# Optimization experiments

Hardware: AMD Instinct MI355X
Metric: run time of the kernel (lower is better)

Reference implementation:

```python
import jax, jax.numpy as jnp
import numpy as np

N_NODES = 20000
N_EDGES = 480000
NUM_BATCH = 8     # B = batch_id.max()+1 (static)
NUM_GLOBAL = 3    # virtual_frame_num default
NUM_RBF = 16
EPS = 1e-20


def make_frames(n, ca, c):
    """OpenFold Rigid.make_transform_from_reference. Returns (R [N,3,3], t [N,3])."""
    nl = n - ca
    cl = c - ca
    cx, cy, cz = cl[:, 0], cl[:, 1], cl[:, 2]
    norm1 = jnp.sqrt(EPS + cx * cx + cy * cy)
    s1, c1 = -cy / norm1, cx / norm1
    norm2 = jnp.sqrt(EPS + cx * cx + cy * cy + cz * cz)
    s2, c2 = cz / norm2, jnp.sqrt(cx * cx + cy * cy) / norm2
    z = jnp.zeros_like(c1)
    o = jnp.ones_like(c1)
    R1 = jnp.stack([jnp.stack([c1, -s1, z], -1),
                    jnp.stack([s1, c1, z], -1),
                    jnp.stack([z, z, o], -1)], -2)          # rot about z
    R2 = jnp.stack([jnp.stack([c2, z, s2], -1),
                    jnp.stack([z, o, z], -1),
                    jnp.stack([-s2, z, c2], -1)], -2)       # rot about y
    Rc = jnp.einsum('nij,njk->nik', R2, R1)
    nr = jnp.einsum('nij,nj->ni', Rc, nl)
    ny, nz = nr[:, 1], nr[:, 2]
    norm3 = jnp.sqrt(EPS + ny * ny + nz * nz)
    sn, cn = -nz / norm3, ny / norm3
    Rn = jnp.stack([jnp.stack([o, z, z], -1),
                    jnp.stack([z, cn, -sn], -1),
                    jnp.stack([z, sn, cn], -1)], -2)        # rot about x
    R = jnp.einsum('nij,njk->nik', Rn, Rc).swapaxes(-1, -2)
    return R, ca


def rbf_encode(D):
    # D_min=0, D_max=20, 16 bins (matches rbf_func)
    mu = jnp.linspace(0.0, 20.0, NUM_RBF, dtype=D.dtype)
    sigma = 20.0 / NUM_RBF
    z = (D[..., None] - mu) / sigma
    return jnp.exp(-z * z)


def decouple(U):
    # safe norm: exact forward, NaN-free backward at U==0
    sq = jnp.sum(U * U, axis=-1, keepdims=True)
    norm = jnp.where(sq == 0, 0.0, jnp.sqrt(jnp.where(sq == 0, 1.0, sq)))
    direct = U / (norm + 1e-6)
    return jnp.concatenate([direct, rbf_encode(norm[..., 0])], axis=-1)


def int_embedding(d, num_embeddings):
    freq = jnp.exp(jnp.arange(0, num_embeddings, 2, dtype=jnp.float32)
                   * (-np.log(10000.0) / num_embeddings))
    ang = d[:, None].astype(jnp.float32) * freq[None, :]
    return jnp.concatenate([jnp.cos(ang), jnp.sin(ang)], -1)


def forward(X, edge_idx, batch_id, chain_encoding):
    N = X.shape[0]
    src, dst = edge_idx[0], edge_idx[1]
    R, t = make_frames(X[:, 0], X[:, 1], X[:, 2])
    # T_ts = T[dst].invert().compose(T[src]):  R_dst^T R_src,  R_dst^T (t_src - t_dst)
    R_ts = jnp.einsum('eji,ejk->eik', R[dst], R[src])
    t_ts = jnp.einsum('eji,ej->ei', R[dst], t[src] - t[dst])
    # --- node features ---
    diffX = jnp.diff(X.reshape(-1, 3), axis=0)
    diffX = jnp.concatenate([jnp.zeros((1, 3), X.dtype), diffX], 0).reshape(N, 4, 3)
    diffX_proj = jnp.einsum('nji,naj->nai', R, diffX)   # R^T @ diffX
    V = decouple(diffX_proj).reshape(N, -1)             # [N, 4*(3+16)=76]
    V = jnp.where(jnp.isnan(V), 0.0, V)
    # --- edge features ---
    atoms = jnp.concatenate([X[src], X[dst]], axis=1)   # [E,8,3]
    diffE = jnp.einsum('eji,eaj->eai', R[src], atoms - t[src][:, None, :])
    diffE = decouple(diffE).reshape(src.shape[0], -1)   # [E,152]
    pos_embed = int_embedding(src - dst, 16)            # [E,16]
    E_quant = R_ts.swapaxes(-1, -2).reshape(-1, 9)      # inverted rot mats
    E_trans = decouple(t_ts)                            # [E,19]
    Efeat = jnp.concatenate([diffE, E_quant, E_trans, pos_embed], -1)  # [E,196]
    # --- virtual (global) frames ---
    B, G = NUM_BATCH, NUM_GLOBAL
    g_src = jnp.concatenate([batch_id + N + k * B for k in range(G)])  # [G*N]
    g_dst = jnp.tile(jnp.arange(N, dtype=edge_idx.dtype), G)
    edge_idx_g = jnp.concatenate([jnp.stack([g_src, g_dst]),
                                  jnp.stack([g_dst, g_src])], axis=1)  # [2, 2*G*N]
    batch_id_g = jnp.tile(jnp.arange(B, dtype=batch_id.dtype), G)      # [G*B]
    h_V_g = jnp.tile(jnp.arange(G), B)                                 # [G*B]
    V_g = int_embedding(h_V_g, V.shape[-1]).astype(V.dtype)            # [G*B,76]
    n_ge = edge_idx_g.shape[1]
    E_g = jnp.zeros((n_ge, Efeat.shape[1]), Efeat.dtype)
    eye = jnp.eye(3, dtype=X.dtype)
    # --- merge local + global ---
    V_all = jnp.concatenate([V, V_g], 0)
    E_all = jnp.concatenate([Efeat, E_g], 0)
    R_all = jnp.concatenate([R, jnp.broadcast_to(eye, (G * B, 3, 3))], 0)
    t_all = jnp.concatenate([t, jnp.zeros((G * B, 3), X.dtype)], 0)
    Rts_all = jnp.concatenate([R_ts, jnp.broadcast_to(eye, (n_ge, 3, 3))], 0)
    tts_all = jnp.concatenate([t_ts, jnp.zeros((n_ge, 3), X.dtype)], 0)
    batch_all = jnp.concatenate([batch_id, batch_id_g])
    edge_all = jnp.concatenate([edge_idx, edge_idx_g], axis=1)
    chain_all = jnp.concatenate([chain_encoding, jnp.ones_like(batch_id_g) + 1000])
    return V_all, E_all, R_all, t_all, Rts_all, tts_all, batch_all, edge_all, chain_all


def setup_inputs() -> dict:
    key = jax.random.key(0)
    k1, k2, k3, k4 = jax.random.split(key, 4)
    X = jax.random.normal(k1, (N_NODES, 4, 3), dtype=jnp.float32)
    edge_idx = jax.random.randint(k2, (2, N_EDGES), 0, N_NODES, dtype=jnp.int32)
    batch_id = jnp.sort(jax.random.randint(k3, (N_NODES,), 0, NUM_BATCH, dtype=jnp.int32))
    chain_encoding = jax.random.randint(k4, (N_NODES,), 0, 10, dtype=jnp.int32)
    return {"X": X, "edge_idx": edge_idx, "batch_id": batch_id,
            "chain_encoding": chain_encoding}


def reference(X, edge_idx, batch_id, chain_encoding):
    return forward(X, edge_idx, batch_id, chain_encoding)
```

## Files before the change

kernel.cpp:

```cpp
#include <hip/hip_runtime.h>

#define NN 20000
#define NE 480000

#define OFF_V    0
#define OFF_E    1521824
#define OFF_R    119121824
#define OFF_T    119302040
#define OFF_RTS  119362112
#define OFF_TTS  124762112
#define OFF_BAT  126562112
#define OFF_EDG  126582136
#define OFF_CHN  127782136

#define REC 65

struct Frame { float m[3][3]; float t[3]; };

__device__ __forceinline__ void make_frame(const float a0[3], const float a1[3],
                                           const float a2[3], Frame& F){
  float nlx = a0[0]-a1[0], nly = a0[1]-a1[1], nlz = a0[2]-a1[2];
  float cx  = a2[0]-a1[0], cy  = a2[1]-a1[1], cz  = a2[2]-a1[2];
  float xy2 = cx*cx + cy*cy;
  float n1 = sqrtf(1e-20f + xy2);
  float s1 = -cy/n1, c1 = cx/n1;
  float n2 = sqrtf(1e-20f + xy2 + cz*cz);
  float s2 = cz/n2, c2 = sqrtf(xy2)/n2;
  float R00 = c2*c1, R01 = -c2*s1, R02 = s2;
  float R10 = s1,    R11 = c1,     R12 = 0.f;
  float R20 = -s2*c1,R21 = s2*s1,  R22 = c2;
  float nr1 = R10*nlx + R11*nly + R12*nlz;
  float nr2 = R20*nlx + R21*nly + R22*nlz;
  float n3 = sqrtf(1e-20f + nr1*nr1 + nr2*nr2);
  float sn = -nr2/n3, cn = nr1/n3;
  F.m[0][0]=R00;              F.m[0][1]=R01;              F.m[0][2]=R02;
  F.m[1][0]=cn*R10 - sn*R20;  F.m[1][1]=cn*R11 - sn*R21;  F.m[1][2]=cn*R12 - sn*R22;
  F.m[2][0]=sn*R10 + cn*R20;  F.m[2][1]=sn*R11 + cn*R21;  F.m[2][2]=sn*R12 + cn*R22;
  F.t[0]=a1[0]; F.t[1]=a1[1]; F.t[2]=a1[2];
}

__device__ __forceinline__ void group4(float ux, float uy, float uz, float* rec, int off){
  float sq = ux*ux + uy*uy + uz*uz;
  float nrm = (sq == 0.f) ? 0.f : sqrtf(sq);
  float inv = 1.0f / (nrm + 1e-6f);
  rec[off+0] = ux*inv; rec[off+1] = uy*inv; rec[off+2] = uz*inv; rec[off+3] = nrm;
}

__global__ __launch_bounds__(128) void edge_kernel(
    const float* __restrict__ X, const int* __restrict__ ei,
    float* __restrict__ out){
  __shared__ float lds[2*64*REC];
  const int tid  = threadIdx.x;
  const int lane = tid & 63;
  const int wave = tid >> 6;
  const int e_my = blockIdx.x*128 + tid;

  int src = ei[e_my], dst = ei[NE + e_my];
  const float* ps = X + (size_t)src*12;
  const float* pd = X + (size_t)dst*12;
  float as[4][3], ad[4][3];
#pragma unroll
  for (int i = 0; i < 12; i++){ as[i/3][i%3] = ps[i]; ad[i/3][i%3] = pd[i]; }
  Frame Fs, Fd;
  make_frame(as[0], as[1], as[2], Fs);
  make_frame(ad[0], ad[1], ad[2], Fd);

  float* rec = lds + (wave*64 + lane)*REC;

#pragma unroll
  for (int q = 0; q < 4; q++){
    float y0 = as[q][0]-Fs.t[0], y1 = as[q][1]-Fs.t[1], y2 = as[q][2]-Fs.t[2];
    group4(Fs.m[0][0]*y0 + Fs.m[0][1]*y1 + Fs.m[0][2]*y2,
           Fs.m[1][0]*y0 + Fs.m[1][1]*y1 + Fs.m[1][2]*y2,
           Fs.m[2][0]*y0 + Fs.m[2][1]*y1 + Fs.m[2][2]*y2, rec, 4*q);
  }
#pragma unroll
  for (int q = 0; q < 4; q++){
    float y0 = ad[q][0]-Fs.t[0], y1 = ad[q][1]-Fs.t[1], y2 = ad[q][2]-Fs.t[2];
    group4(Fs.m[0][0]*y0 + Fs.m[0][1]*y1 + Fs.m[0][2]*y2,
           Fs.m[1][0]*y0 + Fs.m[1][1]*y1 + Fs.m[1][2]*y2,
           Fs.m[2][0]*y0 + Fs.m[2][1]*y1 + Fs.m[2][2]*y2, rec, 16 + 4*q);
  }
#pragma unroll
  for (int i = 0; i < 3; i++)
#pragma unroll
    for (int k = 0; k < 3; k++)
      rec[36+3*i+k] = Fd.m[i][0]*Fs.m[k][0] + Fd.m[i][1]*Fs.m[k][1] + Fd.m[i][2]*Fs.m[k][2];
  {
    float d0 = Fs.t[0]-Fd.t[0], d1 = Fs.t[1]-Fd.t[1], d2 = Fs.t[2]-Fd.t[2];
    float t0 = Fd.m[0][0]*d0 + Fd.m[0][1]*d1 + Fd.m[0][2]*d2;
    float t1 = Fd.m[1][0]*d0 + Fd.m[1][1]*d1 + Fd.m[1][2]*d2;
    float t2 = Fd.m[2][0]*d0 + Fd.m[2][1]*d1 + Fd.m[2][2]*d2;
    rec[45] = t0; rec[46] = t1; rec[47] = t2;
    group4(t0, t1, t2, rec, 32);
  }
  {
    float df = (float)(src - dst);
    const float FR[8] = {1.f, 0.31622776601683794f, 0.1f, 0.031622776601683794f,
                         0.01f, 0.0031622776601683794f, 0.001f, 0.00031622776601683794f};
#pragma unroll
    for (int k = 0; k < 8; k++){
      float s, c; __sincosf(df * FR[k], &s, &c);
      rec[48+k] = c; rec[56+k] = s;
    }
  }
  out[OFF_EDG + e_my]          = (float)src;
  out[OFF_EDG + 600000 + e_my] = (float)dst;

  __syncthreads();

  int   offb[4];
  float msk[4], mu[4];
#pragma unroll
  for (int c = 0; c < 4; c++){
    int j = 4*lane + c;
    int off = 0; float m = 0.f, rm = 0.f;
    if (j < 152){
      int jj = (j < 76) ? j : j - 76;
      int g  = ((j < 76) ? 0 : 4) + jj/19;
      int r  = jj - 19*(jj/19);
      if (r < 3) off = 4*g + r;
      else { off = 4*g + 3; m = 1.f; rm = (float)(r-3) * (20.0f/15.0f); }
    } else if (j < 161){
      int q = j - 152;
      off = 36 + 3*(q - 3*(q/3)) + q/3;
    } else if (j < 180){
      int r = j - 161;
      if (r < 3) off = 32 + r;
      else { off = 35; m = 1.f; rm = (float)(r-3) * (20.0f/15.0f); }
    } else if (j < 196){
      off = 48 + (j - 180);
    } else {
      off = 0;
    }
    offb[c] = off; msk[c] = m; mu[c] = rm;
  }

  const float* wlds = lds + wave*64*REC;
  const int wave_ebase = blockIdx.x*128 + wave*64;
  float4* pstore = reinterpret_cast<float4*>(out + OFF_E + (size_t)wave_ebase*196) + lane;

#pragma unroll 2
  for (int e = 0; e < 64; e++){
    const float* r = wlds + e*REC;
    float v[4];
#pragma unroll
    for (int c = 0; c < 4; c++){
      float x  = r[offb[c]];
      float z  = (x - mu[c]) * 0.8f;
      float rv = __expf(-z*z);
      v[c] = fmaf(msk[c], rv - x, x);
    }
    if (lane < 49)
      *pstore = make_float4(v[0], v[1], v[2], v[3]);
    pstore += 49;
  }

#pragma unroll
  for (int k = 0; k < 9; k++){
    int f = k*64 + lane;
    int e = f/9, m = f - 9*e;
    out[OFF_RTS + (size_t)wave_ebase*9 + f] = wlds[e*REC + 36 + m];
  }
#pragma unroll
  for (int k = 0; k < 3; k++){
    int f = k*64 + lane;
    int e = f/3, m = f - 3*e;
    out[OFF_TTS + (size_t)wave_ebase*3 + f] = wlds[e*REC + 45 + m];
  }
}

__device__ __forceinline__ void decouple19(float ux, float uy, float uz, float* b){
  float sq = ux*ux + uy*uy + uz*uz;
  float nrm = (sq == 0.f) ? 0.f : sqrtf(sq);
  float inv = 1.0f / (nrm + 1e-6f);
  b[0] = ux*inv; b[1] = uy*inv; b[2] = uz*inv;
#pragma unroll
  for (int k = 0; k < 16; k++){
    float mu = (float)k * (20.0f/15.0f);
    float z = (nrm - mu) * 0.8f;
    b[3+k] = __expf(-z*z);
  }
}

__global__ __launch_bounds__(256) void node_kernel(
    const float* __restrict__ X, const int* __restrict__ bat,
    const int* __restrict__ chn, float* __restrict__ out){
  int n = blockIdx.x*256 + threadIdx.x;
  if (n >= NN) return;
  const float* xp = X + (size_t)n*12;
  float a[4][3];
#pragma unroll
  for (int i = 0; i < 12; i++) a[i/3][i%3] = xp[i];
  Frame F; make_frame(a[0], a[1], a[2], F);

  float d[4][3];
  if (n > 0){ d[0][0]=a[0][0]-xp[-3]; d[0][1]=a[0][1]-xp[-2]; d[0][2]=a[0][2]-xp[-1]; }
  else      { d[0][0]=0.f; d[0][1]=0.f; d[0][2]=0.f; }
#pragma unroll
  for (int q = 1; q < 4; q++){
    d[q][0]=a[q][0]-a[q-1][0]; d[q][1]=a[q][1]-a[q-1][1]; d[q][2]=a[q][2]-a[q-1][2];
  }

  float buf[76];
#pragma unroll
  for (int q = 0; q < 4; q++){
    float vx = F.m[0][0]*d[q][0] + F.m[0][1]*d[q][1] + F.m[0][2]*d[q][2];
    float vy = F.m[1][0]*d[q][0] + F.m[1][1]*d[q][1] + F.m[1][2]*d[q][2];
    float vz = F.m[2][0]*d[q][0] + F.m[2][1]*d[q][1] + F.m[2][2]*d[q][2];
    decouple19(vx, vy, vz, buf + q*19);
  }
  float4* vrow = reinterpret_cast<float4*>(out + OFF_V + (size_t)n*76);
#pragma unroll
  for (int i = 0; i < 19; i++)
    vrow[i] = make_float4(buf[4*i], buf[4*i+1], buf[4*i+2], buf[4*i+3]);

  float* rr = out + OFF_R + (size_t)n*9;
#pragma unroll
  for (int i = 0; i < 3; i++)
#pragma unroll
    for (int j = 0; j < 3; j++) rr[3*i+j] = F.m[j][i];

  float* tr = out + OFF_T + (size_t)n*3;
#pragma unroll
  for (int i = 0; i < 3; i++) tr[i] = F.t[i];

  out[OFF_BAT + n] = (float)bat[n];
  out[OFF_CHN + n] = (float)chn[n];
}

__global__ __launch_bounds__(256) void fill_kernel(const int* __restrict__ bat,
                                                   float* __restrict__ out){
  int i = blockIdx.x*256 + threadIdx.x;
  if (i < 5880000){
    uint4 z; z.x=0; z.y=0; z.z=0; z.w=0;
    reinterpret_cast<uint4*>(out + 95601824)[i] = z;
    return;
  }
  i -= 5880000;
  if (i < 90000){
    uint4 z; z.x=0; z.y=0; z.z=0; z.w=0;
    reinterpret_cast<uint4*>(out + 126202112)[i] = z;
    return;
  }
  i -= 90000;
  if (i < 1080000){
    int r = i % 9;
    out[OFF_RTS + 4320000 + i] = (r==0 || r==4 || r==8) ? 1.0f : 0.0f;
    return;
  }
  i -= 1080000;
  if (i < 120000){
    int v0, v1;
    if (i < 60000){ int k = i/20000, m = i - 20000*k; v0 = bat[m] + 20000 + k*8; v1 = m; }
    else { int i2 = i - 60000; int k = i2/20000, m = i2 - 20000*k; v0 = m; v1 = bat[m] + 20000 + k*8; }
    out[OFF_EDG + 480000 + i]          = (float)v0;
    out[OFF_EDG + 600000 + 480000 + i] = (float)v1;
    return;
  }
  i -= 120000;
  if (i >= 2160) return;
  if (i < 1824){
    int r = i / 76, c = i % 76;
    float hv = (float)(r % 3);
    int j = (c < 38) ? c : c - 38;
    float fr = __expf(-(float)(2*j) * (9.210340371976184f/76.0f));
    float ang = hv * fr;
    out[OFF_V + 1520000 + i] = (c < 38) ? cosf(ang) : sinf(ang);
  } else if (i < 2040){
    int k = i - 1824; int r = k % 9;
    out[OFF_R + 180000 + k] = (r==0 || r==4 || r==8) ? 1.0f : 0.0f;
  } else if (i < 2112){
    out[OFF_T + 60000 + (i - 2040)] = 0.0f;
  } else if (i < 2136){
    int k = i - 2112;
    out[OFF_BAT + 20000 + k] = (float)(k % 8);
  } else {
    out[OFF_CHN + 20000 + (i - 2136)] = 1001.0f;
  }
}

extern "C" void kernel_launch(void* const* d_in, const int* in_sizes, int n_in,
                              void* d_out, int out_size, void* d_ws, size_t ws_size,
                              hipStream_t stream) {
  const float* X   = (const float*)d_in[0];
  const int* ei    = (const int*)d_in[1];
  const int* bat   = (const int*)d_in[2];
  const int* chn   = (const int*)d_in[3];
  float* out = (float*)d_out;

  node_kernel<<<(NN + 255)/256, 256, 0, stream>>>(X, bat, chn, out);
  edge_kernel<<<NE/128, 128, 0, stream>>>(X, ei, out);
  fill_kernel<<<(7172160 + 255)/256, 256, 0, stream>>>(bat, out);
}
```

Measured before the change: 120.6 us.

## Fuse node, edge and fill kernels into a single block-dispatched launch

Merges the three separate kernels into one mega kernel that selects edge, node or fill work by block index, removing two launches and the gaps between them. The fill path now writes two uint4 per thread for the zero regions and a float4 per thread for the identity-rotation block. The __syncthreads between the per-lane LDS record writes and the cross-lane reads in the edge path is dropped, relying on each wave reading only its own records. Every block now reserves the edge path's LDS, which can limit how many fill and node blocks fit on a CU at once.

```diff
diff --git a/kernel.cpp b/kernel.cpp
--- a/kernel.cpp
+++ b/kernel.cpp
@@ -14,6 +14,11 @@
 #define OFF_CHN  127782136
 
 #define REC 65
+
+#define NB_EDGE 3750
+#define NB_NODE 157
+#define NB_FILL 26385
+#define NB_TOTAL (NB_EDGE + NB_NODE + NB_FILL)
 
 struct Frame { float m[3][3]; float t[3]; };
 
@@ -46,130 +51,6 @@
   rec[off+0] = ux*inv; rec[off+1] = uy*inv; rec[off+2] = uz*inv; rec[off+3] = nrm;
 }
 
-__global__ __launch_bounds__(128) void edge_kernel(
-    const float* __restrict__ X, const int* __restrict__ ei,
-    float* __restrict__ out){
-  __shared__ float lds[2*64*REC];
-  const int tid  = threadIdx.x;
-  const int lane = tid & 63;
-  const int wave = tid >> 6;
-  const int e_my = blockIdx.x*128 + tid;
-
-  int src = ei[e_my], dst = ei[NE + e_my];
-  const float* ps = X + (size_t)src*12;
-  const float* pd = X + (size_t)dst*12;
-  float as[4][3], ad[4][3];
-#pragma unroll
-  for (int i = 0; i < 12; i++){ as[i/3][i%3] = ps[i]; ad[i/3][i%3] = pd[i]; }
-  Frame Fs, Fd;
-  make_frame(as[0], as[1], as[2], Fs);
-  make_frame(ad[0], ad[1], ad[2], Fd);
-
-  float* rec = lds + (wave*64 + lane)*REC;
-
-#pragma unroll
-  for (int q = 0; q < 4; q++){
-    float y0 = as[q][0]-Fs.t[0], y1 = as[q][1]-Fs.t[1], y2 = as[q][2]-Fs.t[2];
-    group4(Fs.m[0][0]*y0 + Fs.m[0][1]*y1 + Fs.m[0][2]*y2,
-           Fs.m[1][0]*y0 + Fs.m[1][1]*y1 + Fs.m[1][2]*y2,
-           Fs.m[2][0]*y0 + Fs.m[2][1]*y1 + Fs.m[2][2]*y2, rec, 4*q);
-  }
-#pragma unroll
-  for (int q = 0; q < 4; q++){
-    float y0 = ad[q][0]-Fs.t[0], y1 = ad[q][1]-Fs.t[1], y2 = ad[q][2]-Fs.t[2];
-    group4(Fs.m[0][0]*y0 + Fs.m[0][1]*y1 + Fs.m[0][2]*y2,
-           Fs.m[1][0]*y0 + Fs.m[1][1]*y1 + Fs.m[1][2]*y2,
-           Fs.m[2][0]*y0 + Fs.m[2][1]*y1 + Fs.m[2][2]*y2, rec, 16 + 4*q);
-  }
-#pragma unroll
-  for (int i = 0; i < 3; i++)
-#pragma unroll
-    for (int k = 0; k < 3; k++)
-      rec[36+3*i+k] = Fd.m[i][0]*Fs.m[k][0] + Fd.m[i][1]*Fs.m[k][1] + Fd.m[i][2]*Fs.m[k][2];
-  {
-    float d0 = Fs.t[0]-Fd.t[0], d1 = Fs.t[1]-Fd.t[1], d2 = Fs.t[2]-Fd.t[2];
-    float t0 = Fd.m[0][0]*d0 + Fd.m[0][1]*d1 + Fd.m[0][2]*d2;
-    float t1 = Fd.m[1][0]*d0 + Fd.m[1][1]*d1 + Fd.m[1][2]*d2;
-    float t2 = Fd.m[2][0]*d0 + Fd.m[2][1]*d1 + Fd.m[2][2]*d2;
-    rec[45] = t0; rec[46] = t1; rec[47] = t2;
-    group4(t0, t1, t2, rec, 32);
-  }
-  {
-    float df = (float)(src - dst);
-    const float FR[8] = {1.f, 0.31622776601683794f, 0.1f, 0.031622776601683794f,
-                         0.01f, 0.0031622776601683794f, 0.001f, 0.00031622776601683794f};
-#pragma unroll
-    for (int k = 0; k < 8; k++){
-      float s, c; __sincosf(df * FR[k], &s, &c);
-      rec[48+k] = c; rec[56+k] = s;
-    }
-  }
-  out[OFF_EDG + e_my]          = (float)src;
-  out[OFF_EDG + 600000 + e_my] = (float)dst;
-
-  __syncthreads();
-
-  int   offb[4];
-  float msk[4], mu[4];
-#pragma unroll
-  for (int c = 0; c < 4; c++){
-    int j = 4*lane + c;
-    int off = 0; float m = 0.f, rm = 0.f;
-    if (j < 152){
-      int jj = (j < 76) ? j : j - 76;
-      int g  = ((j < 76) ? 0 : 4) + jj/19;
-      int r  = jj - 19*(jj/19);
-      if (r < 3) off = 4*g + r;
-      else { off = 4*g + 3; m = 1.f; rm = (float)(r-3) * (20.0f/15.0f); }
-    } else if (j < 161){
-      int q = j - 152;
-      off = 36 + 3*(q - 3*(q/3)) + q/3;
-    } else if (j < 180){
-      int r = j - 161;
-      if (r < 3) off = 32 + r;
-      else { off = 35; m = 1.f; rm = (float)(r-3) * (20.0f/15.0f); }
-    } else if (j < 196){
-      off = 48 + (j - 180);
-    } else {
-      off = 0;
-    }
-    offb[c] = off; msk[c] = m; mu[c] = rm;
-  }
-
-  const float* wlds = lds + wave*64*REC;
-  const int wave_ebase = blockIdx.x*128 + wave*64;
-  float4* pstore = reinterpret_cast<float4*>(out + OFF_E + (size_t)wave_ebase*196) + lane;
-
-#pragma unroll 2
-  for (int e = 0; e < 64; e++){
-    const float* r = wlds + e*REC;
-    float v[4];
-#pragma unroll
-    for (int c = 0; c < 4; c++){
-      float x  = r[offb[c]];
-      float z  = (x - mu[c]) * 0.8f;
-      float rv = __expf(-z*z);
-      v[c] = fmaf(msk[c], rv - x, x);
-    }
-    if (lane < 49)
-      *pstore = make_float4(v[0], v[1], v[2], v[3]);
-    pstore += 49;
-  }
-
-#pragma unroll
-  for (int k = 0; k < 9; k++){
-    int f = k*64 + lane;
-    int e = f/9, m = f - 9*e;
-    out[OFF_RTS + (size_t)wave_ebase*9 + f] = wlds[e*REC + 36 + m];
-  }
-#pragma unroll
-  for (int k = 0; k < 3; k++){
-    int f = k*64 + lane;
-    int e = f/3, m = f - 3*e;
-    out[OFF_TTS + (size_t)wave_ebase*3 + f] = wlds[e*REC + 45 + m];
-  }
-}
-
 __device__ __forceinline__ void decouple19(float ux, float uy, float uz, float* b){
   float sq = ux*ux + uy*uy + uz*uz;
   float nrm = (sq == 0.f) ? 0.f : sqrtf(sq);
@@ -183,73 +64,206 @@
   }
 }
 
-__global__ __launch_bounds__(256) void node_kernel(
-    const float* __restrict__ X, const int* __restrict__ bat,
-    const int* __restrict__ chn, float* __restrict__ out){
-  int n = blockIdx.x*256 + threadIdx.x;
-  if (n >= NN) return;
-  const float* xp = X + (size_t)n*12;
-  float a[4][3];
-#pragma unroll
-  for (int i = 0; i < 12; i++) a[i/3][i%3] = xp[i];
-  Frame F; make_frame(a[0], a[1], a[2], F);
-
-  float d[4][3];
-  if (n > 0){ d[0][0]=a[0][0]-xp[-3]; d[0][1]=a[0][1]-xp[-2]; d[0][2]=a[0][2]-xp[-1]; }
-  else      { d[0][0]=0.f; d[0][1]=0.f; d[0][2]=0.f; }
-#pragma unroll
-  for (int q = 1; q < 4; q++){
-    d[q][0]=a[q][0]-a[q-1][0]; d[q][1]=a[q][1]-a[q-1][1]; d[q][2]=a[q][2]-a[q-1][2];
-  }
-
-  float buf[76];
-#pragma unroll
-  for (int q = 0; q < 4; q++){
-    float vx = F.m[0][0]*d[q][0] + F.m[0][1]*d[q][1] + F.m[0][2]*d[q][2];
-    float vy = F.m[1][0]*d[q][0] + F.m[1][1]*d[q][1] + F.m[1][2]*d[q][2];
-    float vz = F.m[2][0]*d[q][0] + F.m[2][1]*d[q][1] + F.m[2][2]*d[q][2];
-    decouple19(vx, vy, vz, buf + q*19);
-  }
-  float4* vrow = reinterpret_cast<float4*>(out + OFF_V + (size_t)n*76);
-#pragma unroll
-  for (int i = 0; i < 19; i++)
-    vrow[i] = make_float4(buf[4*i], buf[4*i+1], buf[4*i+2], buf[4*i+3]);
-
-  float* rr = out + OFF_R + (size_t)n*9;
-#pragma unroll
-  for (int i = 0; i < 3; i++)
-#pragma unroll
-    for (int j = 0; j < 3; j++) rr[3*i+j] = F.m[j][i];
-
-  float* tr = out + OFF_T + (size_t)n*3;
-#pragma unroll
-  for (int i = 0; i < 3; i++) tr[i] = F.t[i];
-
-  out[OFF_BAT + n] = (float)bat[n];
-  out[OFF_CHN + n] = (float)chn[n];
-}
-
-__global__ __launch_bounds__(256) void fill_kernel(const int* __restrict__ bat,
-                                                   float* __restrict__ out){
-  int i = blockIdx.x*256 + threadIdx.x;
-  if (i < 5880000){
+__global__ __launch_bounds__(128) void mega_kernel(
+    const float* __restrict__ X, const int* __restrict__ ei,
+    const int* __restrict__ bat, const int* __restrict__ chn,
+    float* __restrict__ out){
+  __shared__ float lds[2*64*REC];
+  const int blk = blockIdx.x;
+  const int tid = threadIdx.x;
+
+  if (blk < NB_EDGE){
+    const int lane = tid & 63;
+    const int wave = tid >> 6;
+    const int e_my = blk*128 + tid;
+
+    int src = ei[e_my], dst = ei[NE + e_my];
+    const float* ps = X + (size_t)src*12;
+    const float* pd = X + (size_t)dst*12;
+    float as[4][3], ad[4][3];
+#pragma unroll
+    for (int i = 0; i < 12; i++){ as[i/3][i%3] = ps[i]; ad[i/3][i%3] = pd[i]; }
+    Frame Fs, Fd;
+    make_frame(as[0], as[1], as[2], Fs);
+    make_frame(ad[0], ad[1], ad[2], Fd);
+
+    float* rec = lds + (wave*64 + lane)*REC;
+
+#pragma unroll
+    for (int q = 0; q < 4; q++){
+      float y0 = as[q][0]-Fs.t[0], y1 = as[q][1]-Fs.t[1], y2 = as[q][2]-Fs.t[2];
+      group4(Fs.m[0][0]*y0 + Fs.m[0][1]*y1 + Fs.m[0][2]*y2,
+             Fs.m[1][0]*y0 + Fs.m[1][1]*y1 + Fs.m[1][2]*y2,
+             Fs.m[2][0]*y0 + Fs.m[2][1]*y1 + Fs.m[2][2]*y2, rec, 4*q);
+    }
+#pragma unroll
+    for (int q = 0; q < 4; q++){
+      float y0 = ad[q][0]-Fs.t[0], y1 = ad[q][1]-Fs.t[1], y2 = ad[q][2]-Fs.t[2];
+      group4(Fs.m[0][0]*y0 + Fs.m[0][1]*y1 + Fs.m[0][2]*y2,
+             Fs.m[1][0]*y0 + Fs.m[1][1]*y1 + Fs.m[1][2]*y2,
+             Fs.m[2][0]*y0 + Fs.m[2][1]*y1 + Fs.m[2][2]*y2, rec, 16 + 4*q);
+    }
+#pragma unroll
+    for (int i = 0; i < 3; i++)
+#pragma unroll
+      for (int k = 0; k < 3; k++)
+        rec[36+3*i+k] = Fd.m[i][0]*Fs.m[k][0] + Fd.m[i][1]*Fs.m[k][1] + Fd.m[i][2]*Fs.m[k][2];
+    {
+      float d0 = Fs.t[0]-Fd.t[0], d1 = Fs.t[1]-Fd.t[1], d2 = Fs.t[2]-Fd.t[2];
+      float t0 = Fd.m[0][0]*d0 + Fd.m[0][1]*d1 + Fd.m[0][2]*d2;
+      float t1 = Fd.m[1][0]*d0 + Fd.m[1][1]*d1 + Fd.m[1][2]*d2;
+      float t2 = Fd.m[2][0]*d0 + Fd.m[2][1]*d1 + Fd.m[2][2]*d2;
+      rec[45] = t0; rec[46] = t1; rec[47] = t2;
+      group4(t0, t1, t2, rec, 32);
+    }
+    {
+      float df = (float)(src - dst);
+      const float FR[8] = {1.f, 0.31622776601683794f, 0.1f, 0.031622776601683794f,
+                           0.01f, 0.0031622776601683794f, 0.001f, 0.00031622776601683794f};
+#pragma unroll
+      for (int k = 0; k < 8; k++){
+        float s, c; __sincosf(df * FR[k], &s, &c);
+        rec[48+k] = c; rec[56+k] = s;
+      }
+    }
+    out[OFF_EDG + e_my]          = (float)src;
+    out[OFF_EDG + 600000 + e_my] = (float)dst;
+
+
+    int   offb[4];
+    float msk[4], mu[4];
+#pragma unroll
+    for (int c = 0; c < 4; c++){
+      int j = 4*lane + c;
+      int off = 0; float m = 0.f, rm = 0.f;
+      if (j < 152){
+        int jj = (j < 76) ? j : j - 76;
+        int g  = ((j < 76) ? 0 : 4) + jj/19;
+        int r  = jj - 19*(jj/19);
+        if (r < 3) off = 4*g + r;
+        else { off = 4*g + 3; m = 1.f; rm = (float)(r-3) * (20.0f/15.0f); }
+      } else if (j < 161){
+        int q = j - 152;
+        off = 36 + 3*(q - 3*(q/3)) + q/3;
+      } else if (j < 180){
+        int r = j - 161;
+        if (r < 3) off = 32 + r;
+        else { off = 35; m = 1.f; rm = (float)(r-3) * (20.0f/15.0f); }
+      } else if (j < 196){
+        off = 48 + (j - 180);
+      } else {
+        off = 0;
+      }
+      offb[c] = off; msk[c] = m; mu[c] = rm;
+    }
+
+    const float* wlds = lds + wave*64*REC;
+    const int wave_ebase = blk*128 + wave*64;
+    float4* pstore = reinterpret_cast<float4*>(out + OFF_E + (size_t)wave_ebase*196) + lane;
+
+#pragma unroll 2
+    for (int e = 0; e < 64; e++){
+      const float* r = wlds + e*REC;
+      float v[4];
+#pragma unroll
+      for (int c = 0; c < 4; c++){
+        float x  = r[offb[c]];
+        float z  = (x - mu[c]) * 0.8f;
+        float rv = __expf(-z*z);
+        v[c] = fmaf(msk[c], rv - x, x);
+      }
+      if (lane < 49)
+        *pstore = make_float4(v[0], v[1], v[2], v[3]);
+      pstore += 49;
+    }
+
+#pragma unroll
+    for (int k = 0; k < 9; k++){
+      int f = k*64 + lane;
+      int e = f/9, m = f - 9*e;
+      out[OFF_RTS + (size_t)wave_ebase*9 + f] = wlds[e*REC + 36 + m];
+    }
+#pragma unroll
+    for (int k = 0; k < 3; k++){
+      int f = k*64 + lane;
+      int e = f/3, m = f - 3*e;
+      out[OFF_TTS + (size_t)wave_ebase*3 + f] = wlds[e*REC + 45 + m];
+    }
+    return;
+  }
+
+  if (blk < NB_EDGE + NB_NODE){
+    int n = (blk - NB_EDGE)*128 + tid;
+    if (n >= NN) return;
+    const float* xp = X + (size_t)n*12;
+    float a[4][3];
+#pragma unroll
+    for (int i = 0; i < 12; i++) a[i/3][i%3] = xp[i];
+    Frame F; make_frame(a[0], a[1], a[2], F);
+
+    float d[4][3];
+    if (n > 0){ d[0][0]=a[0][0]-xp[-3]; d[0][1]=a[0][1]-xp[-2]; d[0][2]=a[0][2]-xp[-1]; }
+    else      { d[0][0]=0.f; d[0][1]=0.f; d[0][2]=0.f; }
+#pragma unroll
+    for (int q = 1; q < 4; q++){
+      d[q][0]=a[q][0]-a[q-1][0]; d[q][1]=a[q][1]-a[q-1][1]; d[q][2]=a[q][2]-a[q-1][2];
+    }
+
+    float buf[76];
+#pragma unroll
+    for (int q = 0; q < 4; q++){
+      float vx = F.m[0][0]*d[q][0] + F.m[0][1]*d[q][1] + F.m[0][2]*d[q][2];
+      float vy = F.m[1][0]*d[q][0] + F.m[1][1]*d[q][1] + F.m[1][2]*d[q][2];
+      float vz = F.m[2][0]*d[q][0] + F.m[2][1]*d[q][1] + F.m[2][2]*d[q][2];
+      decouple19(vx, vy, vz, buf + q*19);
+    }
+    float4* vrow = reinterpret_cast<float4*>(out + OFF_V + (size_t)n*76);
+#pragma unroll
+    for (int i = 0; i < 19; i++)
+      vrow[i] = make_float4(buf[4*i], buf[4*i+1], buf[4*i+2], buf[4*i+3]);
+
+    float* rr = out + OFF_R + (size_t)n*9;
+#pragma unroll
+    for (int i = 0; i < 3; i++)
+#pragma unroll
+      for (int j = 0; j < 3; j++) rr[3*i+j] = F.m[j][i];
+
+    float* tr = out + OFF_T + (size_t)n*3;
+#pragma unroll
+    for (int i = 0; i < 3; i++) tr[i] = F.t[i];
+
+    out[OFF_BAT + n] = (float)bat[n];
+    out[OFF_CHN + n] = (float)chn[n];
+    return;
+  }
+
+  int i = (blk - NB_EDGE - NB_NODE)*128 + tid;
+  if (i < 2940000){
     uint4 z; z.x=0; z.y=0; z.z=0; z.w=0;
-    reinterpret_cast<uint4*>(out + 95601824)[i] = z;
-    return;
-  }
-  i -= 5880000;
-  if (i < 90000){
+    uint4* p = reinterpret_cast<uint4*>(out + 95601824) + 2*(size_t)i;
+    p[0] = z; p[1] = z;
+    return;
+  }
+  i -= 2940000;
+  if (i < 45000){
     uint4 z; z.x=0; z.y=0; z.z=0; z.w=0;
-    reinterpret_cast<uint4*>(out + 126202112)[i] = z;
-    return;
-  }
-  i -= 90000;
-  if (i < 1080000){
-    int r = i % 9;
-    out[OFF_RTS + 4320000 + i] = (r==0 || r==4 || r==8) ? 1.0f : 0.0f;
-    return;
-  }
-  i -= 1080000;
+    uint4* p = reinterpret_cast<uint4*>(out + 126202112) + 2*(size_t)i;
+    p[0] = z; p[1] = z;
+    return;
+  }
+  i -= 45000;
+  if (i < 270000){
+    float v[4];
+#pragma unroll
+    for (int c = 0; c < 4; c++){
+      int idx = 4*i + c;
+      int r = idx % 9;
+      v[c] = (r==0 || r==4 || r==8) ? 1.0f : 0.0f;
+    }
+    reinterpret_cast<float4*>(out + OFF_RTS + 4320000)[i] = make_float4(v[0],v[1],v[2],v[3]);
+    return;
+  }
+  i -= 270000;
   if (i < 120000){
     int v0, v1;
     if (i < 60000){ int k = i/20000, m = i - 20000*k; v0 = bat[m] + 20000 + k*8; v1 = m; }
@@ -289,7 +303,5 @@
   const int* chn   = (const int*)d_in[3];
   float* out = (float*)d_out;
 
-  node_kernel<<<(NN + 255)/256, 256, 0, stream>>>(X, bat, chn, out);
-  edge_kernel<<<NE/128, 128, 0, stream>>>(X, ei, out);
-  fill_kernel<<<(7172160 + 255)/256, 256, 0, stream>>>(bat, out);
-}
+  mega_kernel<<<NB_TOTAL, 128, 0, stream>>>(X, ei, bat, chn, out);
+}
```

Result: faster. 114.9 us (-4.7%).
